# Kernel optimization log

Hardware: AMD Instinct MI355X
Metric: run time of the kernel (lower is better)

## Reference

```python
import jax, jax.numpy as jnp
import numpy as np

B, S, IN_DIM, OUT_DIM = 32, 2048, 1024, 1024


def setup_inputs() -> dict:
    key = jax.random.key(0)
    k1, k2, k3, k4, k5, k6 = jax.random.split(key, 6)
    k = jax.random.normal(k1, (B, IN_DIM), dtype=jnp.float32)
    xs = jax.random.normal(k2, (B, S, OUT_DIM), dtype=jnp.float32)
    mask = jax.random.randint(k3, (B, S), 0, 2).astype(jnp.bool_)
    # learned params (nn.Linear stores weight as [out, in]; y = x @ W.T)
    Wa = jax.random.normal(k4, (OUT_DIM, IN_DIM), dtype=jnp.float32) * (IN_DIM ** -0.5)
    Wb = jax.random.normal(k5, (OUT_DIM, OUT_DIM), dtype=jnp.float32) * (OUT_DIM ** -0.5)
    energy = jax.random.normal(k6, (OUT_DIM,), dtype=jnp.float32)
    return {"k": k, "xs": xs, "mask": mask, "Wa": Wa, "Wb": Wb, "energy": energy}


def reference(k, xs, mask, Wa, Wb, energy):
    # Wa(k): [B, out]; broadcast over S instead of materializing repeated ks
    a = jnp.einsum('bi,oi->bo', k, Wa)            # [B, out]
    b = jnp.einsum('bsj,oj->bso', xs, Wb)         # [B, S, out]
    w = jnp.tanh(a[:, None, :] + b)               # [B, S, out]
    scores = jnp.einsum('bso,o->bs', w, energy)   # [B, S]
    scores = jnp.where(mask, scores, -jnp.inf)
    attn = jax.nn.softmax(scores, axis=-1)        # [B, S]
    ctx = jnp.einsum('bs,bsd->bd', attn, xs)      # [B, out]
    return ctx, attn
```

## Files before the change

kernel.cpp:

```cpp
#include <hip/hip_runtime.h>
#include <hip/hip_bf16.h>

#define NB 32
#define NS 2048
#define DIM 1024
#define NM (NB*NS)
#define CAP 256
#define SEL_MARGIN 24.0f

typedef __attribute__((ext_vector_type(8))) short short8;
typedef __attribute__((ext_vector_type(4))) float f32x4;
typedef __attribute__((ext_vector_type(4))) unsigned short us16x4;
typedef unsigned short us16;
typedef unsigned int   u32;
typedef __attribute__((address_space(3))) void lds_void;
typedef __attribute__((address_space(1))) void glb_void;

__device__ __forceinline__ void gload16(const void* g, void* l){
  __builtin_amdgcn_global_load_lds((const glb_void*)g, (lds_void*)l, 16, 0, 0);
}

__device__ __forceinline__ float fast_tanh(float x){
  float e = __builtin_exp2f(x * 2.8853900817779268f);
  return 1.0f - 2.0f/(e + 1.0f);
}

__device__ __forceinline__ void split_bf16(float x, short &hi, short &lo){
  u32 u = __float_as_uint(x);
  float hf = __uint_as_float(u & 0xFFFF0000u);
  hi = (short)(u >> 16);
  lo = (short)(__float_as_uint(x - hf) >> 16);
}

__global__ void k_prep(const float* __restrict__ wb,
                       const float* __restrict__ kin,
                       const float* __restrict__ wa,
                       const int* __restrict__ mask,
                       char* __restrict__ imgf,
                       char* __restrict__ img1,
                       float* __restrict__ avec,
                       int* __restrict__ cidx,
                       int* __restrict__ cnt,
                       int* __restrict__ sel_count){
  __shared__ float4 kl[256];
  __shared__ int tc[256];
  __shared__ int tot;
  const int h = blockIdx.x, t = threadIdx.x;
  if(h == 0 && t < NB) sel_count[t] = 0;
  if(h < 1024){
    const int tid = h*256 + t;
    const int kt   = tid >> 13;
    const int ct16 = (tid >> 7) & 63;
    const int hl   = (tid >> 6) & 1;
    const int lane = tid & 63;
    const int col  = ct16*16 + (lane & 15);
    const int k0   = kt*32 + (lane >> 4)*8;
    const float* src = wb + (size_t)col*DIM + k0;
    float4 v0 = *(const float4*)src;
    float4 v1 = *(const float4*)(src + 4);
    float fv[8] = {v0.x,v0.y,v0.z,v0.w,v1.x,v1.y,v1.z,v1.w};
    short8 out;
    #pragma unroll
    for(int j=0;j<8;j++){
      short hi,lo; split_bf16(fv[j],hi,lo);
      out[j] = hl ? lo : hi;
    }
    *(short8*)(imgf + (size_t)tid*16) = out;
  } else if(h < 1536){
    const int tid = (h-1024)*256 + t;
    const int tile = tid >> 10;
    const int kt = tile >> 2, cb = tile & 3;
    const int byt = (tid & 1023) * 16;
    const int row = byt >> 7, inner = byt & 127;
    const int ix = inner ^ ((row & 7) << 4);
    const int colhi = ix >> 6, lkk = (ix >> 4) & 3;
    const int col = cb*256 + colhi*128 + row;
    const float* src = wb + (size_t)col*DIM + kt*32 + lkk*8;
    float4 v0 = *(const float4*)src;
    float4 v1 = *(const float4*)(src + 4);
    float fv[8] = {v0.x,v0.y,v0.z,v0.w,v1.x,v1.y,v1.z,v1.w};
    short8 out;
    #pragma unroll
    for(int j=0;j<8;j++) out[j] = (short)(__float_as_uint(fv[j]) >> 16);
    *(short8*)(img1 + (size_t)tid*16) = out;
  } else if(h < 1664){
    const int hb = h - 1536;
    const int b = hb >> 2, oc = hb & 3;
    kl[t] = *(const float4*)(kin + b*DIM + t*4);
    __syncthreads();
    const int o = oc*256 + t;
    const float4* wrow = (const float4*)(wa + (size_t)o*DIM);
    float acc = 0.f;
    for(int i=0;i<256;i++){
      float4 wv = wrow[i]; float4 kk = kl[i];
      acc += wv.x*kk.x + wv.y*kk.y + wv.z*kk.z + wv.w*kk.w;
    }
    avec[b*DIM + o] = acc;
  } else {
    const int b = h - 1664;
    int mv[8]; int c = 0;
    #pragma unroll
    for(int e=0;e<8;e++){ mv[e] = mask[b*NS + t*8 + e]; c += (mv[e] ? 1 : 0); }
    tc[t] = c;
    __syncthreads();
    for(int d=1; d<256; d<<=1){
      int v = tc[t];
      int add = (t >= d) ? tc[t-d] : 0;
      __syncthreads();
      tc[t] = v + add;
      __syncthreads();
    }
    const int excl = tc[t] - c;
    if(t == 255) tot = tc[t];
    __syncthreads();
    int pos = excl;
    #pragma unroll
    for(int e=0;e<8;e++){
      if(mv[e]) cidx[b*NS + (pos++)] = t*8 + e;
    }
    const int total = tot;
    if(t == 0) cnt[b] = total;
    for(int p = total + t; p < NS; p += 256) cidx[b*NS + p] = 0;
  }
}

__global__ __launch_bounds__(256,2)
void k_gemm_approx(const float* __restrict__ xs,
                   const char* __restrict__ img1,
                   const float* __restrict__ avec,
                   const float* __restrict__ energy,
                   const int* __restrict__ cidx,
                   const int* __restrict__ cnt,
                   float* __restrict__ partial){
  __shared__ us16 Abuf[128][40];
  __shared__ us16 Bbuf[2][128][64];

  const int h = blockIdx.x;
  int bidx, tile, cb;
  if(h < 1152){
    const int q = h >> 3;
    cb = q & 3;
    const int pair = (h & 7)*36 + (q >> 2);
    bidx = pair / 9; tile = pair % 9;
  } else {
    const int h2 = h - 1152;
    bidx = h2 / 28; tile = 9 + ((h2 % 28) >> 2); cb = h2 & 3;
  }
  if(tile*128 >= cnt[bidx]) return;
  const int t  = threadIdx.x;
  const int w  = t >> 6, lane = t & 63;
  const int wr = w >> 1, wc = w & 1;
  const int lm = lane & 15, lk = lane >> 4;
  const int sr = t >> 1, sh = t & 1;

  const int orig = cidx[bidx*NS + tile*128 + sr];
  const float* ap = xs + ((size_t)bidx*NS + orig)*DIM + sh*16;
  const char*  bsrc = img1;

  const char* a_rd = (const char*)&Abuf[0][0] + (wr*64 + lm)*80 + ((lk*16) ^ ((lm&3)<<4));
  const int boff = (wc*64 + lk*16) ^ ((lm&7)<<4);

  f32x4 acc[4][8];
  #pragma unroll
  for(int m=0;m<4;m++)
    #pragma unroll
    for(int n=0;n<8;n++) acc[m][n] = (f32x4){0.f,0.f,0.f,0.f};

  float4 ar0 = *(const float4*)(ap+0),  ar1 = *(const float4*)(ap+4);
  float4 ar2 = *(const float4*)(ap+8),  ar3 = *(const float4*)(ap+12);
  {
    const char* gs = bsrc + (size_t)cb*16384 + t*16;
    char* ld = (char*)&Bbuf[0][0][0] + t*16;
    #pragma unroll
    for(int c=0;c<4;c++) gload16(gs + c*4096, ld + c*4096);
  }

  for(int kt=0; kt<32; kt++){
    const int cur = kt & 1;
    asm volatile("s_waitcnt lgkmcnt(0)" ::: "memory");
    __builtin_amdgcn_sched_barrier(0);
    __builtin_amdgcn_s_barrier();
    {
      float fv[16];
      *(float4*)(fv+0)=ar0; *(float4*)(fv+4)=ar1;
      *(float4*)(fv+8)=ar2; *(float4*)(fv+12)=ar3;
      short8 h0, h1;
      #pragma unroll
      for(int j=0;j<8;j++){ h0[j] = (short)(__float_as_uint(fv[j])>>16);
                            h1[j] = (short)(__float_as_uint(fv[8+j])>>16); }
      char* abase = (char*)&Abuf[0][0] + sr*80;
      const int swz = (sr & 3) << 4;
      *(short8*)(abase + ((sh*32     ) ^ swz)) = h0;
      *(short8*)(abase + ((sh*32 + 16) ^ swz)) = h1;
    }
    if(kt < 31){
      const float* a2 = ap + (kt+1)*32;
      ar0 = *(const float4*)(a2+0);  ar1 = *(const float4*)(a2+4);
      ar2 = *(const float4*)(a2+8);  ar3 = *(const float4*)(a2+12);
      {
        const char* gs = bsrc + (size_t)((kt+1)*4 + cb)*16384 + t*16;
        char* ld = (char*)&Bbuf[cur^1][0][0] + t*16;
        #pragma unroll
        for(int c=0;c<4;c++) gload16(gs + c*4096, ld + c*4096);
      }
      asm volatile("s_waitcnt vmcnt(8) lgkmcnt(0)" ::: "memory");
    } else {
      asm volatile("s_waitcnt vmcnt(0) lgkmcnt(0)" ::: "memory");
    }
    __builtin_amdgcn_sched_barrier(0);
    __builtin_amdgcn_s_barrier();

    short8 fa[4], fb[8];
    const char* bb = (const char*)&Bbuf[cur][0][0] + lm*128 + boff;
    #pragma unroll
    for(int m=0;m<4;m++) fa[m] = *(const short8*)(a_rd + m*1280);
    #pragma unroll
    for(int n=0;n<8;n++) fb[n] = *(const short8*)(bb + n*2048);
    #pragma unroll
    for(int m=0;m<4;m++)
      #pragma unroll
      for(int n=0;n<8;n++)
        acc[m][n] = __builtin_amdgcn_mfma_f32_16x16x32_bf16(fa[m], fb[n], acc[m][n], 0,0,0);
  }

  float av[8], ev[8];
  #pragma unroll
  for(int n=0;n<8;n++){
    const int col = cb*256 + wc*128 + n*16 + lm;
    av[n] = avec[bidx*DIM + col];
    ev[n] = energy[col];
  }
  #pragma unroll
  for(int m=0;m<4;m++){
    float rs[4];
    #pragma unroll
    for(int j=0;j<4;j++){
      float s = 0.f;
      #pragma unroll
      for(int n=0;n<8;n++) s += ev[n]*fast_tanh(av[n] + acc[m][n][j]);
      s += __shfl_xor(s,1); s += __shfl_xor(s,2);
      s += __shfl_xor(s,4); s += __shfl_xor(s,8);
      rs[j] = s;
    }
    if(lm == 0){
      float4 st = {rs[0], rs[1], rs[2], rs[3]};
      *(float4*)(partial + (size_t)(cb*2+wc)*NM + bidx*NS + tile*128 + wr*64 + m*16 + lk*4) = st;
    }
  }
}

__global__ void k_select(const float* __restrict__ partial,
                         const int* __restrict__ cidx,
                         const int* __restrict__ cnt,
                         float* __restrict__ scores,
                         int* __restrict__ sel_count,
                         int* __restrict__ sel_list){
  const int b = blockIdx.x, t = threadIdx.x;
  const int w = t >> 6, lane = t & 63;
  __shared__ float red[4];
  const int cnt_b = cnt[b];
  float sv[8]; int orig[8];
  float m = -3.4e38f;
  #pragma unroll
  for(int j=0;j<8;j++){
    const int i = j*256 + t;
    if(i < cnt_b){
      float s = 0.f;
      #pragma unroll
      for(int c=0;c<8;c++) s += partial[(size_t)c*NM + b*NS + i];
      sv[j] = s;
      orig[j] = cidx[b*NS + i];
      scores[b*NS + orig[j]] = s;
      if(s > m) m = s;
    } else { sv[j] = -3.4e38f; orig[j] = -1; }
  }
  #pragma unroll
  for(int off=1; off<64; off<<=1) m = fmaxf(m, __shfl_xor(m, off));
  if(lane==0) red[w] = m;
  __syncthreads();
  m = fmaxf(fmaxf(red[0],red[1]), fmaxf(red[2],red[3]));
  const float thr = m - SEL_MARGIN;
  #pragma unroll
  for(int j=0;j<8;j++){
    if(orig[j] >= 0 && sv[j] > thr){
      int slot = atomicAdd(&sel_count[b], 1);
      if(slot < CAP) sel_list[b*CAP + slot] = orig[j];
    }
  }
}

__global__ __launch_bounds__(256)
void k_phase2(const float* __restrict__ xs,
              const char* __restrict__ imgf,
              const float* __restrict__ avec,
              const float* __restrict__ energy,
              const int* __restrict__ sel_count,
              const int* __restrict__ sel_list,
              float* __restrict__ p2buf){
  __shared__ us16 A2[32][80];
  __shared__ float s2[4][32];
  const int b = blockIdx.x >> 4, cb = blockIdx.x & 15;
  const int t = threadIdx.x, w = t >> 6, lane = t & 63;
  const int lm = lane & 15, lk = lane >> 4;
  const int ct = cb*4 + w;
  const int col = ct*16 + lm;
  const float av  = avec[b*DIM + col];
  const float evv = energy[col];
  char* lds = (char*)&A2[0][0];
  const int count = min(sel_count[b], CAP);
  const int ri = t >> 3, seg = t & 7;
  const int wbyte = ri*160 + ((seg*8) ^ ((ri&3)<<4));
  const char* a_rd = lds + lm*160 + ((lk*16) ^ ((lm&3)<<4));

  for(int c0 = 0; c0 < count; c0 += 32){
    const int li = c0 + ri;
    const int row = sel_list[b*CAP + min(li, count-1)];
    const float* rp = xs + ((size_t)b*NS + row)*DIM + seg*4;
    f32x4 acc[2];
    acc[0] = (f32x4){0.f,0.f,0.f,0.f};
    acc[1] = (f32x4){0.f,0.f,0.f,0.f};
    for(int kt=0; kt<32; kt++){
      __syncthreads();
      float4 v = *(const float4*)(rp + kt*32);
      float fv[4] = {v.x, v.y, v.z, v.w};
      us16x4 hi, lo;
      #pragma unroll
      for(int e=0;e<4;e++){
        short a, l; split_bf16(fv[e], a, l);
        hi[e] = (us16)a; lo[e] = (us16)l;
      }
      *(us16x4*)(lds + wbyte)      = hi;
      *(us16x4*)(lds + wbyte + 80) = lo;
      __syncthreads();
      const char* fbb = imgf + ((size_t)(kt*64 + ct)*2)*1024 + lane*16;
      short8 bh = *(const short8*)(fbb);
      short8 bl = *(const short8*)(fbb + 1024);
      short8 fah[2], fal[2];
      #pragma unroll
      for(int m=0;m<2;m++){
        fah[m] = *(const short8*)(a_rd + m*2560);
        fal[m] = *(const short8*)(a_rd + m*2560 + 80);
      }
      #pragma unroll
      for(int m=0;m<2;m++)
        acc[m] = __builtin_amdgcn_mfma_f32_16x16x32_bf16(fah[m], bh, acc[m], 0,0,0);
      #pragma unroll
      for(int m=0;m<2;m++)
        acc[m] = __builtin_amdgcn_mfma_f32_16x16x32_bf16(fah[m], bl, acc[m], 0,0,0);
      #pragma unroll
      for(int m=0;m<2;m++)
        acc[m] = __builtin_amdgcn_mfma_f32_16x16x32_bf16(fal[m], bh, acc[m], 0,0,0);
    }
    float s[2][4];
    #pragma unroll
    for(int m=0;m<2;m++)
      #pragma unroll
      for(int j=0;j<4;j++){
        float v = evv * fast_tanh(av + acc[m][j]);
        v += __shfl_xor(v,1); v += __shfl_xor(v,2);
        v += __shfl_xor(v,4); v += __shfl_xor(v,8);
        s[m][j] = v;
      }
    __syncthreads();
    if(lm == 0){
      #pragma unroll
      for(int m=0;m<2;m++)
        #pragma unroll
        for(int j=0;j<4;j++) s2[w][m*16 + lk*4 + j] = s[m][j];
    }
    __syncthreads();
    if(t < 32){
      float sum = s2[0][t] + s2[1][t] + s2[2][t] + s2[3][t];
      p2buf[((size_t)b*16 + cb)*CAP + c0 + t] = sum;
    }
  }
}

__global__ void k_softmax(const float* __restrict__ scores,
                          const float* __restrict__ p2buf,
                          const int* __restrict__ sel_count,
                          const int* __restrict__ sel_list,
                          const int* __restrict__ mask,
                          float* __restrict__ attn,
                          int* __restrict__ slist2,
                          float* __restrict__ sval2,
                          int* __restrict__ scount2){
  const int b = blockIdx.x, t = threadIdx.x;
  const int w = t >> 6, lane = t & 63;
  __shared__ float sc[NS];
  __shared__ float red[4];
  __shared__ int tc[256];
  __shared__ int tot;
  #pragma unroll
  for(int j=0;j<8;j++) sc[j*256+t] = scores[b*NS + j*256 + t];
  __syncthreads();
  const int count = min(sel_count[b], CAP);
  for(int s0 = t; s0 < count; s0 += 256){
    float s = 0.f;
    #pragma unroll
    for(int c=0;c<16;c++) s += p2buf[((size_t)b*16 + c)*CAP + s0];
    sc[sel_list[b*CAP + s0]] = s;
  }
  __syncthreads();
  float sv[8]; int mv[8];
  float m = -3.4e38f;
  #pragma unroll
  for(int j=0;j<8;j++){
    const int i = j*256 + t;
    sv[j] = sc[i];
    mv[j] = mask[b*NS + i];
    if(mv[j] && sv[j] > m) m = sv[j];
  }
  #pragma unroll
  for(int off=1; off<64; off<<=1) m = fmaxf(m, __shfl_xor(m, off));
  if(lane==0) red[w] = m;
  __syncthreads();
  m = fmaxf(fmaxf(red[0],red[1]), fmaxf(red[2],red[3]));
  __syncthreads();
  float ev[8]; float l = 0.f;
  #pragma unroll
  for(int j=0;j<8;j++){
    ev[j] = mv[j] ? __builtin_exp2f((sv[j]-m)*1.4426950408889634f) : 0.f;
    l += ev[j];
  }
  #pragma unroll
  for(int off=1; off<64; off<<=1) l += __shfl_xor(l, off);
  if(lane==0) red[w] = l;
  __syncthreads();
  l = red[0]+red[1]+red[2]+red[3];
  const float inv = 1.0f/l;
  float av8[8]; int sig[8]; int c = 0;
  #pragma unroll
  for(int j=0;j<8;j++){
    av8[j] = ev[j]*inv;
    attn[b*NS + j*256 + t] = av8[j];
    sig[j] = (av8[j] > 1e-9f) ? 1 : 0;
    c += sig[j];
  }
  tc[t] = c;
  __syncthreads();
  for(int d=1; d<256; d<<=1){
    int v = tc[t];
    int add = (t >= d) ? tc[t-d] : 0;
    __syncthreads();
    tc[t] = v + add;
    __syncthreads();
  }
  const int excl = tc[t] - c;
  if(t == 255) tot = tc[t];
  __syncthreads();
  int pos = excl;
  #pragma unroll
  for(int j=0;j<8;j++){
    if(sig[j]){
      slist2[b*NS + pos] = j*256 + t;
      sval2 [b*NS + pos] = av8[j];
      pos++;
    }
  }
  if(t == 0) scount2[b] = tot;
}

__global__ void k_ctx(const int* __restrict__ slist2,
                      const float* __restrict__ sval2,
                      const int* __restrict__ scount2,
                      const float* __restrict__ xs,
                      float* __restrict__ ctx){
  const int b = blockIdx.x >> 2, ch = blockIdx.x & 3;
  const int t = threadIdx.x;
  __shared__ int   rows[NS];
  __shared__ float aw[NS];
  const int n = scount2[b];
  for(int i = t; i < n; i += 256){
    rows[i] = slist2[b*NS + i];
    aw[i]   = sval2 [b*NS + i];
  }
  __syncthreads();
  float acc = 0.f;
  const int col = ch*256 + t;
  const float* xb = xs + (size_t)b*NS*DIM + col;
  for(int j=0;j<n;j++){
    acc += aw[j] * xb[(size_t)rows[j]*DIM];
  }
  ctx[b*DIM + col] = acc;
}

extern "C" void kernel_launch(void* const* d_in, const int* in_sizes, int n_in,
                              void* d_out, int out_size, void* d_ws, size_t ws_size,
                              hipStream_t stream) {
  const float* kin    = (const float*)d_in[0];
  const float* xs     = (const float*)d_in[1];
  const int*   mask   = (const int*)d_in[2];
  const float* wa     = (const float*)d_in[3];
  const float* wb     = (const float*)d_in[4];
  const float* energy = (const float*)d_in[5];
  float* out  = (float*)d_out;
  float* ctx  = out;
  float* attn = out + NB*DIM;

  char* ws = (char*)d_ws;
  float* partial   = (float*)(ws);
  float* avec      = (float*)(ws + 2097152);
  float* scores    = (float*)(ws + 2228224);
  int*   slist2    = (int*)(ws + 2490368);
  float* sval2     = (float*)(ws + 2752512);
  int*   scount2   = (int*)(ws + 3014656);
  char*  imgf      = ws + 3538944;
  char*  img1      = ws + 7733248;
  int*   sel_count = (int*)(ws + 9830400);
  int*   sel_list  = (int*)(ws + 9830528);
  float* p2buf     = (float*)(ws + 9863296);
  int*   cidx      = (int*)(ws + 10387584);
  int*   cnt       = (int*)(ws + 10649728);

  k_prep       <<<1696, 256, 0, stream>>>(wb, kin, wa, mask, imgf, img1, avec,
                                          cidx, cnt, sel_count);
  k_gemm_approx<<<2048, 256, 0, stream>>>(xs, img1, avec, energy, cidx, cnt, partial);
  k_select     <<<NB, 256, 0, stream>>>(partial, cidx, cnt, scores, sel_count, sel_list);
  k_phase2     <<<512, 256, 0, stream>>>(xs, imgf, avec, energy, sel_count, sel_list, p2buf);
  k_softmax    <<<NB, 256, 0, stream>>>(scores, p2buf, sel_count, sel_list, mask, attn,
                                        slist2, sval2, scount2);
  k_ctx        <<<128, 256, 0, stream>>>(slist2, sval2, scount2, xs, ctx);
}
```

Measured before the change: 255.6 us.

## Double-buffer A tile in LDS and prefetch two steps ahead, one barrier per k-step

```diff
diff --git a/kernel.cpp b/kernel.cpp
--- a/kernel.cpp
+++ b/kernel.cpp
@@ -124,6 +124,21 @@
   }
 }
 
+#define SPLIT_STORE_A(DST, AR0,AR1,AR2,AR3)                                     \
+  {                                                                             \
+    float fv[16];                                                               \
+    *(float4*)(fv+0)=AR0; *(float4*)(fv+4)=AR1;                                 \
+    *(float4*)(fv+8)=AR2; *(float4*)(fv+12)=AR3;                                \
+    short8 h0, h1;                                                              \
+    _Pragma("unroll")                                                           \
+    for(int j=0;j<8;j++){ h0[j] = (short)(__float_as_uint(fv[j])>>16);          \
+                          h1[j] = (short)(__float_as_uint(fv[8+j])>>16); }      \
+    char* abase = (DST) + sr*80;                                                \
+    const int swz = (sr & 3) << 4;                                              \
+    *(short8*)(abase + ((sh*32     ) ^ swz)) = h0;                              \
+    *(short8*)(abase + ((sh*32 + 16) ^ swz)) = h1;                              \
+  }
+
 __global__ __launch_bounds__(256,2)
 void k_gemm_approx(const float* __restrict__ xs,
                    const char* __restrict__ img1,
@@ -132,7 +147,7 @@
                    const int* __restrict__ cidx,
                    const int* __restrict__ cnt,
                    float* __restrict__ partial){
-  __shared__ us16 Abuf[128][40];
+  __shared__ us16 Abuf[2][128][40];
   __shared__ us16 Bbuf[2][128][64];
 
   const int h = blockIdx.x;
@@ -157,8 +172,10 @@
   const float* ap = xs + ((size_t)bidx*NS + orig)*DIM + sh*16;
   const char*  bsrc = img1;
 
-  const char* a_rd = (const char*)&Abuf[0][0] + (wr*64 + lm)*80 + ((lk*16) ^ ((lm&3)<<4));
-  const int boff = (wc*64 + lk*16) ^ ((lm&7)<<4);
+  const int a_ro = (wr*64 + lm)*80 + ((lk*16) ^ ((lm&3)<<4));
+  const int b_ro = lm*128 + ((wc*64 + lk*16) ^ ((lm&7)<<4));
+  const char* ab_base = (const char*)&Abuf[0][0][0];
+  const char* bb_base = (const char*)&Bbuf[0][0][0];
 
   f32x4 acc[4][8];
   #pragma unroll
@@ -174,53 +191,52 @@
     #pragma unroll
     for(int c=0;c<4;c++) gload16(gs + c*4096, ld + c*4096);
   }
+  SPLIT_STORE_A((char*)&Abuf[0][0][0], ar0, ar1, ar2, ar3);
+  {
+    const float* a1 = ap + 32;
+    ar0 = *(const float4*)(a1+0);  ar1 = *(const float4*)(a1+4);
+    ar2 = *(const float4*)(a1+8);  ar3 = *(const float4*)(a1+12);
+  }
+  asm volatile("s_waitcnt vmcnt(4) lgkmcnt(0)" ::: "memory");
+  __builtin_amdgcn_sched_barrier(0);
+  __builtin_amdgcn_s_barrier();
 
   for(int kt=0; kt<32; kt++){
     const int cur = kt & 1;
+    if(kt < 31){
+      const char* gs = bsrc + (size_t)((kt+1)*4 + cb)*16384 + t*16;
+      char* ld = (char*)&Bbuf[cur^1][0][0] + t*16;
+      #pragma unroll
+      for(int c=0;c<4;c++) gload16(gs + c*4096, ld + c*4096);
+      SPLIT_STORE_A((char*)&Abuf[cur^1][0][0], ar0, ar1, ar2, ar3);
+    }
+    if(kt < 30){
+      const float* a2 = ap + (kt+2)*32;
+      ar0 = *(const float4*)(a2+0);  ar1 = *(const float4*)(a2+4);
+      ar2 = *(const float4*)(a2+8);  ar3 = *(const float4*)(a2+12);
+    }
+    short8 fa[4], fb[8];
+    const char* ar_ = ab_base + cur*10240 + a_ro;
+    const char* bb_ = bb_base + cur*16384 + b_ro;
+    #pragma unroll
+    for(int m=0;m<4;m++) fa[m] = *(const short8*)(ar_ + m*1280);
+    #pragma unroll
+    for(int n=0;n<8;n++) fb[n] = *(const short8*)(bb_ + n*2048);
     asm volatile("s_waitcnt lgkmcnt(0)" ::: "memory");
     __builtin_amdgcn_sched_barrier(0);
-    __builtin_amdgcn_s_barrier();
-    {
-      float fv[16];
-      *(float4*)(fv+0)=ar0; *(float4*)(fv+4)=ar1;
-      *(float4*)(fv+8)=ar2; *(float4*)(fv+12)=ar3;
-      short8 h0, h1;
-      #pragma unroll
-      for(int j=0;j<8;j++){ h0[j] = (short)(__float_as_uint(fv[j])>>16);
-                            h1[j] = (short)(__float_as_uint(fv[8+j])>>16); }
-      char* abase = (char*)&Abuf[0][0] + sr*80;
-      const int swz = (sr & 3) << 4;
-      *(short8*)(abase + ((sh*32     ) ^ swz)) = h0;
-      *(short8*)(abase + ((sh*32 + 16) ^ swz)) = h1;
-    }
-    if(kt < 31){
-      const float* a2 = ap + (kt+1)*32;
-      ar0 = *(const float4*)(a2+0);  ar1 = *(const float4*)(a2+4);
-      ar2 = *(const float4*)(a2+8);  ar3 = *(const float4*)(a2+12);
-      {
-        const char* gs = bsrc + (size_t)((kt+1)*4 + cb)*16384 + t*16;
-        char* ld = (char*)&Bbuf[cur^1][0][0] + t*16;
-        #pragma unroll
-        for(int c=0;c<4;c++) gload16(gs + c*4096, ld + c*4096);
-      }
-      asm volatile("s_waitcnt vmcnt(8) lgkmcnt(0)" ::: "memory");
-    } else {
-      asm volatile("s_waitcnt vmcnt(0) lgkmcnt(0)" ::: "memory");
-    }
-    __builtin_amdgcn_sched_barrier(0);
-    __builtin_amdgcn_s_barrier();
-
-    short8 fa[4], fb[8];
-    const char* bb = (const char*)&Bbuf[cur][0][0] + lm*128 + boff;
-    #pragma unroll
-    for(int m=0;m<4;m++) fa[m] = *(const short8*)(a_rd + m*1280);
-    #pragma unroll
-    for(int n=0;n<8;n++) fb[n] = *(const short8*)(bb + n*2048);
+    __builtin_amdgcn_s_setprio(1);
     #pragma unroll
     for(int m=0;m<4;m++)
       #pragma unroll
       for(int n=0;n<8;n++)
         acc[m][n] = __builtin_amdgcn_mfma_f32_16x16x32_bf16(fa[m], fb[n], acc[m][n], 0,0,0);
+    __builtin_amdgcn_s_setprio(0);
+    if(kt < 31){
+      if(kt < 30) asm volatile("s_waitcnt vmcnt(4)" ::: "memory");
+      else        asm volatile("s_waitcnt vmcnt(0)" ::: "memory");
+      __builtin_amdgcn_sched_barrier(0);
+      __builtin_amdgcn_s_barrier();
+    }
   }
 
   float av[8], ev[8];
```

New measurement: 254.2 us. Within noise of the previous version (-0.5%).
